# Performance work log

Measured on AMD Instinct MI355X. Metric: run time of the kernel, lower is better.

## Reference

```python
import jax, jax.numpy as jnp
import numpy as np

N_NODES = 50000
N_EDGES = 640000
IN_FEATS = 512
HID = 128
OUT_FEATS = 128
N_GRAPHS = 256


def setup_inputs() -> dict:
    key = jax.random.key(0)
    ks = jax.random.split(key, 7)
    x = jax.random.normal(ks[0], (N_NODES, IN_FEATS), dtype=jnp.float32)
    edge_index = jax.random.randint(ks[1], (2, N_EDGES), 0, N_NODES, dtype=jnp.int32)
    batch = jnp.sort(jax.random.randint(ks[2], (N_NODES,), 0, N_GRAPHS, dtype=jnp.int32))
    W1 = jax.random.normal(ks[3], (IN_FEATS, HID), dtype=jnp.float32) * (1.0 / np.sqrt(IN_FEATS))
    b1 = jnp.zeros((HID,), jnp.float32)
    W2 = jax.random.normal(ks[4], (HID, OUT_FEATS), dtype=jnp.float32) * (1.0 / np.sqrt(HID))
    b2 = jnp.zeros((OUT_FEATS,), jnp.float32)
    return {"x": x, "W1": W1, "b1": b1, "W2": W2, "b2": b2,
            "edge_index": edge_index, "batch": batch}


def reference(x, W1, b1, W2, b2, edge_index, batch):
    N = x.shape[0]
    loop = jnp.arange(N, dtype=edge_index.dtype)
    # PyG GCNConv default: add self-loops, symmetric deg^-1/2 normalization
    row = jnp.concatenate([edge_index[0], loop])  # source
    col = jnp.concatenate([edge_index[1], loop])  # target
    deg = jax.ops.segment_sum(jnp.ones_like(col, x.dtype), col, num_segments=N)
    dinv = jnp.where(deg > 0, jax.lax.rsqrt(deg), 0.0)
    norm = dinv[row] * dinv[col]  # [E+N]

    def gcn_conv(h, W, b):
        h = h @ W  # linear transform first (PyG order)
        msg = h[row] * norm[:, None]  # gather + scale
        agg = jax.ops.segment_sum(msg, col, num_segments=N)  # scatter-add
        return agg + b

    h = jax.nn.relu(gcn_conv(x, W1, b1))  # dropout is identity in eval mode
    h = gcn_conv(h, W2, b2)
    hs = jax.ops.segment_sum(h, batch, num_segments=N_GRAPHS)  # global_add_pool
    return hs, h
```

## Files before the change

kernel.cpp:

```cpp
#include <hip/hip_runtime.h>
#include <hip/hip_bf16.h>

#define N_NODES  50000
#define N_EDGES  640000
#define IN_FEATS 512
#define HID      128
#define OUT_FEATS 128
#define N_GRAPHS 256

#define SCAN_CHUNK 1024
#define SCAN_BLOCKS ((N_NODES + SCAN_CHUNK - 1) / SCAN_CHUNK)

typedef __attribute__((ext_vector_type(8))) short short8;
typedef __attribute__((ext_vector_type(4))) float f32x4;

__device__ __forceinline__ float bf2f(unsigned short u) {
    return __uint_as_float(((unsigned)u) << 16);
}
__device__ __forceinline__ unsigned short f2bf(float f) {
    __hip_bfloat16 h = __float2bfloat16(f);
    return *(unsigned short*)&h;
}


__global__ void k_count(const int* __restrict__ col, int* __restrict__ cnt) {
    int e = blockIdx.x * blockDim.x + threadIdx.x;
    if (e < N_EDGES) atomicAdd(&cnt[col[e]], 1);
}

__global__ __launch_bounds__(256) void k_scan_a(const int* __restrict__ cnt,
                                                int* __restrict__ offs,
                                                int* __restrict__ bsum) {
    __shared__ int sums[256];
    int t = threadIdx.x;
    int base = blockIdx.x * SCAN_CHUNK + t * 4;
    int c0 = 0, c1 = 0, c2 = 0, c3 = 0;
    if (base + 3 < N_NODES) {
        int4 v = *(const int4*)(cnt + base);
        c0 = v.x; c1 = v.y; c2 = v.z; c3 = v.w;
    } else {
        if (base + 0 < N_NODES) c0 = cnt[base + 0];
        if (base + 1 < N_NODES) c1 = cnt[base + 1];
        if (base + 2 < N_NODES) c2 = cnt[base + 2];
    }
    int ts = c0 + c1 + c2 + c3;
    sums[t] = ts;
    __syncthreads();
#pragma unroll
    for (int off = 1; off < 256; off <<= 1) {
        int add = (t >= off) ? sums[t - off] : 0;
        __syncthreads();
        sums[t] += add;
        __syncthreads();
    }
    int ex = sums[t] - ts;
    if (base + 3 < N_NODES) {
        int4 o;
        o.x = ex; o.y = ex + c0; o.z = ex + c0 + c1; o.w = ex + c0 + c1 + c2;
        *(int4*)(offs + base) = o;
    } else {
        if (base + 0 < N_NODES) offs[base + 0] = ex;
        if (base + 1 < N_NODES) offs[base + 1] = ex + c0;
        if (base + 2 < N_NODES) offs[base + 2] = ex + c0 + c1;
    }
    if (t == 255) bsum[blockIdx.x] = sums[255];
}

__global__ void k_scan_b(int* __restrict__ bsum, int* __restrict__ boff) {
    __shared__ int s[64];
    int t = threadIdx.x;
    int v = (t < SCAN_BLOCKS) ? bsum[t] : 0;
    s[t] = v;
    __syncthreads();
#pragma unroll
    for (int off = 1; off < 64; off <<= 1) {
        int add = (t >= off) ? s[t - off] : 0;
        __syncthreads();
        s[t] += add;
        __syncthreads();
    }
    if (t < SCAN_BLOCKS) boff[t] = s[t] - v;
}

__global__ __launch_bounds__(256) void k_scan_c(const int* __restrict__ cnt,
                                                const int* __restrict__ boff,
                                                int* __restrict__ offs,
                                                int* __restrict__ cursor,
                                                float* __restrict__ dinv) {
    int t = threadIdx.x;
    int b = blockIdx.x;
    int add = boff[b];
    int base = b * SCAN_CHUNK + t * 4;
    if (base + 3 < N_NODES) {
        int4 o = *(const int4*)(offs + base);
        o.x += add; o.y += add; o.z += add; o.w += add;
        *(int4*)(offs + base) = o;
        *(int4*)(cursor + base) = o;
        int4 c = *(const int4*)(cnt + base);
        float4 d;
        d.x = rsqrtf((float)c.x + 1.0f);
        d.y = rsqrtf((float)c.y + 1.0f);
        d.z = rsqrtf((float)c.z + 1.0f);
        d.w = rsqrtf((float)c.w + 1.0f);
        *(float4*)(dinv + base) = d;
    } else {
#pragma unroll
        for (int j = 0; j < 4; ++j) {
            int i = base + j;
            if (i < N_NODES) {
                int o = offs[i] + add;
                offs[i] = o; cursor[i] = o;
                dinv[i] = rsqrtf((float)cnt[i] + 1.0f);
            }
        }
    }
    if (b == 0 && t == 0) offs[N_NODES] = N_EDGES;
}

__global__ void k_fill(const int* __restrict__ row, const int* __restrict__ col,
                       int* __restrict__ cursor, int* __restrict__ srcIdx) {
    int e = blockIdx.x * blockDim.x + threadIdx.x;
    if (e < N_EDGES) {
        int c = col[e];
        int p = atomicAdd(&cursor[c], 1);
        srcIdx[p] = row[e];
    }
}


template <int K>
__global__ void k_cvt_wt(const float* __restrict__ W, unsigned short* __restrict__ Wt) {
    int idx = blockIdx.x * blockDim.x + threadIdx.x;
    if (idx >= K * 128) return;
    int n = idx & 127;
    int k = idx >> 7;
    Wt[(size_t)n * K + k] = f2bf(W[(size_t)k * 128 + n]);
}


template <int K>
__global__ __launch_bounds__(256) void k_gemm_mfma_f32a(const float* __restrict__ A,
                                                        const unsigned short* __restrict__ Bt,
                                                        unsigned short* __restrict__ Cb, int M) {
    __shared__ unsigned short As[4][64][8];
    __shared__ unsigned short Bs[4][128][8];
    int tid = threadIdx.x;
    int wave = tid >> 6;
    int lane = tid & 63;
    int quad = lane >> 4;
    int l15 = lane & 15;
    int m0 = blockIdx.x * 64;

    f32x4 acc[8];
#pragma unroll
    for (int nt = 0; nt < 8; ++nt) acc[nt] = (f32x4){0.f, 0.f, 0.f, 0.f};

    int gm_a = m0 + lane; if (gm_a >= M) gm_a = M - 1;
    const float* ap_base = A + (size_t)gm_a * K + wave * 8;

    for (int k0 = 0; k0 < K; k0 += 32) {
        {
            const float* ap = ap_base + k0;
            float4 v0 = *(const float4*)ap;
            float4 v1 = *(const float4*)(ap + 4);
            float f[8] = {v0.x, v0.y, v0.z, v0.w, v1.x, v1.y, v1.z, v1.w};
            short8 pk;
#pragma unroll
            for (int j = 0; j < 8; ++j) pk[j] = (short)f2bf(f[j]);
            *(short8*)&As[wave][lane][0] = pk;
        }
#pragma unroll
        for (int i = 0; i < 2; ++i) {
            int slot = tid + i * 256;
            int bkq = slot >> 7;
            int n = slot & 127;
            short8 bv = *(const short8*)(Bt + (size_t)n * K + k0 + bkq * 8);
            *(short8*)&Bs[bkq][n][0] = bv;
        }
        __syncthreads();
        short8 a = *(short8*)&As[quad][wave * 16 + l15][0];
#pragma unroll
        for (int nt = 0; nt < 8; ++nt) {
            short8 b = *(short8*)&Bs[quad][nt * 16 + l15][0];
            acc[nt] = __builtin_amdgcn_mfma_f32_16x16x32_bf16(a, b, acc[nt], 0, 0, 0);
        }
        __syncthreads();
    }
    int row_base = m0 + wave * 16 + quad * 4;
#pragma unroll
    for (int nt = 0; nt < 8; ++nt) {
#pragma unroll
        for (int r2 = 0; r2 < 4; ++r2) {
            int gm = row_base + r2;
            if (gm < M) Cb[(size_t)gm * 128 + nt * 16 + l15] = f2bf(acc[nt][r2]);
        }
    }
}


template <int K>
__global__ __launch_bounds__(256) void k_gemm_mfma_bf16a(const unsigned short* __restrict__ A,
                                                         const unsigned short* __restrict__ Bt,
                                                         unsigned short* __restrict__ Cb, int M) {
    __shared__ unsigned short As[4][64][8];
    __shared__ unsigned short Bs[4][128][8];
    int tid = threadIdx.x;
    int wave = tid >> 6;
    int lane = tid & 63;
    int quad = lane >> 4;
    int l15 = lane & 15;
    int m0 = blockIdx.x * 64;

    f32x4 acc[8];
#pragma unroll
    for (int nt = 0; nt < 8; ++nt) acc[nt] = (f32x4){0.f, 0.f, 0.f, 0.f};

    int gm_a = m0 + lane; if (gm_a >= M) gm_a = M - 1;
    const unsigned short* ap_base = A + (size_t)gm_a * K + wave * 8;

    for (int k0 = 0; k0 < K; k0 += 32) {
        *(short8*)&As[wave][lane][0] = *(const short8*)(ap_base + k0);
#pragma unroll
        for (int i = 0; i < 2; ++i) {
            int slot = tid + i * 256;
            int bkq = slot >> 7;
            int n = slot & 127;
            *(short8*)&Bs[bkq][n][0] = *(const short8*)(Bt + (size_t)n * K + k0 + bkq * 8);
        }
        __syncthreads();
        short8 a = *(short8*)&As[quad][wave * 16 + l15][0];
#pragma unroll
        for (int nt = 0; nt < 8; ++nt) {
            short8 b = *(short8*)&Bs[quad][nt * 16 + l15][0];
            acc[nt] = __builtin_amdgcn_mfma_f32_16x16x32_bf16(a, b, acc[nt], 0, 0, 0);
        }
        __syncthreads();
    }
    int row_base = m0 + wave * 16 + quad * 4;
#pragma unroll
    for (int nt = 0; nt < 8; ++nt) {
#pragma unroll
        for (int r2 = 0; r2 < 4; ++r2) {
            int gm = row_base + r2;
            if (gm < M) Cb[(size_t)gm * 128 + nt * 16 + l15] = f2bf(acc[nt][r2]);
        }
    }
}


template <int RELU, int OUTBF>
__global__ __launch_bounds__(128) void k_agg(const unsigned short* __restrict__ t,
                                             const int* __restrict__ offs,
                                             const int* __restrict__ srcIdx,
                                             const float* __restrict__ dinv,
                                             const float* __restrict__ bias,
                                             void* __restrict__ out_) {
    int i = blockIdx.x;
    int f = threadIdx.x;
    float di = dinv[i];
    float s = bf2f(t[(size_t)i * 128 + f]) * di;
    int lo = offs[i], hi = offs[i + 1];
    int e = lo;
    for (; e + 4 <= hi; e += 4) {
        int s0 = srcIdx[e + 0], s1 = srcIdx[e + 1], s2 = srcIdx[e + 2], s3 = srcIdx[e + 3];
        float d0 = dinv[s0], d1 = dinv[s1], d2 = dinv[s2], d3 = dinv[s3];
        float v0 = bf2f(t[(size_t)s0 * 128 + f]);
        float v1 = bf2f(t[(size_t)s1 * 128 + f]);
        float v2 = bf2f(t[(size_t)s2 * 128 + f]);
        float v3 = bf2f(t[(size_t)s3 * 128 + f]);
        s = fmaf(v0, d0, s); s = fmaf(v1, d1, s);
        s = fmaf(v2, d2, s); s = fmaf(v3, d3, s);
    }
    for (; e < hi; ++e) {
        int sn = srcIdx[e];
        s = fmaf(bf2f(t[(size_t)sn * 128 + f]), dinv[sn], s);
    }
    float v = s * di + bias[f];
    if (RELU) v = fmaxf(v, 0.f);
    if (OUTBF) ((unsigned short*)out_)[(size_t)i * 128 + f] = f2bf(v);
    else       ((float*)out_)[(size_t)i * 128 + f] = v;
}


__global__ void k_gstart(const int* __restrict__ batch, int* __restrict__ gstart) {
    int i = blockIdx.x * blockDim.x + threadIdx.x;
    if (i >= N_NODES) return;
    int b = batch[i];
    int bp = (i == 0) ? -1 : batch[i - 1];
    for (int g = bp + 1; g <= b; ++g) gstart[g] = i;
    if (i == N_NODES - 1) {
        for (int g = b + 1; g <= N_GRAPHS; ++g) gstart[g] = N_NODES;
    }
}

__global__ __launch_bounds__(128) void k_pool(const float* __restrict__ h,
                                              const int* __restrict__ gstart,
                                              float* __restrict__ hs) {
    int g = blockIdx.x >> 2;
    int c = blockIdx.x & 3;
    int f = threadIdx.x;
    int lo = gstart[g], hi = gstart[g + 1];
    int len = hi - lo;
    int chunk = (len + 3) >> 2;
    int r0 = lo + c * chunk;
    int r1 = r0 + chunk; if (r1 > hi) r1 = hi;
    if (r0 >= r1) return;
    float s = 0.f;
    for (int r = r0; r < r1; ++r) s += h[(size_t)r * 128 + f];
    atomicAdd(&hs[(size_t)g * 128 + f], s);
}


extern "C" void kernel_launch(void* const* d_in, const int* in_sizes, int n_in,
                              void* d_out, int out_size, void* d_ws, size_t ws_size,
                              hipStream_t stream) {
    const float* x  = (const float*)d_in[0];
    const float* W1 = (const float*)d_in[1];
    const float* b1 = (const float*)d_in[2];
    const float* W2 = (const float*)d_in[3];
    const float* b2 = (const float*)d_in[4];
    const int*   ei = (const int*)d_in[5];
    const int*   batch = (const int*)d_in[6];
    const int* row = ei;
    const int* col = ei + N_EDGES;

    float* out_hs = (float*)d_out;
    float* out_h  = (float*)d_out + N_GRAPHS * OUT_FEATS;

    char* ws = (char*)d_ws;
    unsigned short* tb   = (unsigned short*)ws;
    unsigned short* h1b  = (unsigned short*)(ws + 12800000);
    unsigned short* tb2  = (unsigned short*)(ws + 25600000);
    float* dinv = (float*)(ws + 38400000);
    int*   cnt    = (int*)(ws + 38600000);
    int*   offs   = (int*)(ws + 38800000);
    int*   cursor = (int*)(ws + 39000016);
    int*   srcIdx = (int*)(ws + 39200016);
    int*   gstart = (int*)(ws + 41760016);
    int*   bsum   = (int*)(ws + 41761056);
    int*   boff   = (int*)(ws + 41761264);
    unsigned short* wt1 = (unsigned short*)(ws + 41761472);
    unsigned short* wt2 = (unsigned short*)(ws + 41892544);

    const int TB = 256;
    hipMemsetAsync(cnt, 0, N_NODES * sizeof(int), stream);
    hipMemsetAsync(out_hs, 0, N_GRAPHS * OUT_FEATS * sizeof(float), stream);
    k_count<<<(N_EDGES + TB - 1) / TB, TB, 0, stream>>>(col, cnt);
    k_scan_a<<<SCAN_BLOCKS, 256, 0, stream>>>(cnt, offs, bsum);
    k_scan_b<<<1, 64, 0, stream>>>(bsum, boff);
    k_scan_c<<<SCAN_BLOCKS, 256, 0, stream>>>(cnt, boff, offs, cursor, dinv);
    k_fill<<<(N_EDGES + TB - 1) / TB, TB, 0, stream>>>(row, col, cursor, srcIdx);
    k_gstart<<<(N_NODES + TB - 1) / TB, TB, 0, stream>>>(batch, gstart);
    k_cvt_wt<IN_FEATS><<<(IN_FEATS * 128 + TB - 1) / TB, TB, 0, stream>>>(W1, wt1);
    k_cvt_wt<HID><<<(HID * 128 + TB - 1) / TB, TB, 0, stream>>>(W2, wt2);

    const int GB = (N_NODES + 63) / 64;
    k_gemm_mfma_f32a<IN_FEATS><<<GB, 256, 0, stream>>>(x, wt1, tb, N_NODES);
    k_agg<1, 1><<<N_NODES, 128, 0, stream>>>(tb, offs, srcIdx, dinv, b1, h1b);
    k_gemm_mfma_bf16a<HID><<<GB, 256, 0, stream>>>(h1b, wt2, tb2, N_NODES);
    k_agg<0, 0><<<N_NODES, 128, 0, stream>>>(tb2, offs, srcIdx, dinv, b2, out_h);
    k_pool<<<N_GRAPHS * 4, 128, 0, stream>>>(out_h, gstart, out_hs);
}
```

Before: 375.8 us.

## Fuse setup kernels, merge scan phases, and widen aggregation to one wave per node

Four small setup launches (gstart, weight conversions, and two memsets) are merged into a single k_prep kernel partitioned by block index. The block-sum scan is folded into k_scan_c, so each block recomputes the 64-entry prefix in shared memory. k_agg now assigns one 64-lane wave per node, with each lane handling two bf16 features via 32-bit loads, and unrolls the neighbor gather by 8 for more memory-level parallelism. The aim is to cut launch overhead and make the gather loads wider, at the cost of redundant scan work per block.

```diff
diff --git a/kernel.cpp b/kernel.cpp
--- a/kernel.cpp
+++ b/kernel.cpp
@@ -14,12 +14,51 @@
 typedef __attribute__((ext_vector_type(8))) short short8;
 typedef __attribute__((ext_vector_type(4))) float f32x4;
 
-__device__ __forceinline__ float bf2f(unsigned short u) {
-    return __uint_as_float(((unsigned)u) << 16);
+__device__ __forceinline__ float bf2f(unsigned u16) {
+    return __uint_as_float(u16 << 16);
 }
 __device__ __forceinline__ unsigned short f2bf(float f) {
     __hip_bfloat16 h = __float2bfloat16(f);
     return *(unsigned short*)&h;
+}
+
+
+#define PREP_BLOCKS 840
+
+__global__ __launch_bounds__(256) void k_prep(const float* __restrict__ W1,
+                                              const float* __restrict__ W2,
+                                              const int* __restrict__ batch,
+                                              unsigned short* __restrict__ wt1,
+                                              unsigned short* __restrict__ wt2,
+                                              int* __restrict__ cnt,
+                                              int* __restrict__ gstart,
+                                              float* __restrict__ hs) {
+    int b = blockIdx.x;
+    int t = threadIdx.x;
+    if (b < 196) {
+        int i = b * 256 + t;
+        if (i < N_NODES) {
+            int bt = batch[i];
+            int bp = (i == 0) ? -1 : batch[i - 1];
+            for (int g = bp + 1; g <= bt; ++g) gstart[g] = i;
+            if (i == N_NODES - 1)
+                for (int g = bt + 1; g <= N_GRAPHS; ++g) gstart[g] = N_NODES;
+        }
+    } else if (b < 392) {
+        int i = (b - 196) * 256 + t;
+        if (i < N_NODES) cnt[i] = 0;
+    } else if (b < 648) {
+        int idx = (b - 392) * 256 + t;
+        int n = idx & 127, k = idx >> 7;
+        wt1[(size_t)n * IN_FEATS + k] = f2bf(W1[(size_t)k * 128 + n]);
+    } else if (b < 712) {
+        int idx = (b - 648) * 256 + t;
+        int n = idx & 127, k = idx >> 7;
+        wt2[(size_t)n * HID + k] = f2bf(W2[(size_t)k * 128 + n]);
+    } else {
+        int idx = (b - 712) * 256 + t;
+        hs[idx] = 0.f;
+    }
 }
 
 
@@ -66,30 +105,25 @@
     if (t == 255) bsum[blockIdx.x] = sums[255];
 }
 
-__global__ void k_scan_b(int* __restrict__ bsum, int* __restrict__ boff) {
-    __shared__ int s[64];
-    int t = threadIdx.x;
-    int v = (t < SCAN_BLOCKS) ? bsum[t] : 0;
-    s[t] = v;
-    __syncthreads();
-#pragma unroll
-    for (int off = 1; off < 64; off <<= 1) {
-        int add = (t >= off) ? s[t - off] : 0;
-        __syncthreads();
-        s[t] += add;
-        __syncthreads();
-    }
-    if (t < SCAN_BLOCKS) boff[t] = s[t] - v;
-}
-
 __global__ __launch_bounds__(256) void k_scan_c(const int* __restrict__ cnt,
-                                                const int* __restrict__ boff,
+                                                const int* __restrict__ bsum,
                                                 int* __restrict__ offs,
                                                 int* __restrict__ cursor,
                                                 float* __restrict__ dinv) {
+    __shared__ int sb[64];
     int t = threadIdx.x;
     int b = blockIdx.x;
-    int add = boff[b];
+    if (t < 64) sb[t] = (t < SCAN_BLOCKS) ? bsum[t] : 0;
+    __syncthreads();
+#pragma unroll
+    for (int off = 1; off < 64; off <<= 1) {
+        int add = 0;
+        if (t < 64 && t >= off) add = sb[t - off];
+        __syncthreads();
+        if (t < 64) sb[t] += add;
+        __syncthreads();
+    }
+    int add = (b == 0) ? 0 : sb[b - 1];
     int base = b * SCAN_CHUNK + t * 4;
     if (base + 3 < N_NODES) {
         int4 o = *(const int4*)(offs + base);
@@ -129,16 +163,6 @@
 
 
 template <int K>
-__global__ void k_cvt_wt(const float* __restrict__ W, unsigned short* __restrict__ Wt) {
-    int idx = blockIdx.x * blockDim.x + threadIdx.x;
-    if (idx >= K * 128) return;
-    int n = idx & 127;
-    int k = idx >> 7;
-    Wt[(size_t)n * K + k] = f2bf(W[(size_t)k * 128 + n]);
-}
-
-
-template <int K>
 __global__ __launch_bounds__(256) void k_gemm_mfma_f32a(const float* __restrict__ A,
                                                         const unsigned short* __restrict__ Bt,
                                                         unsigned short* __restrict__ Cb, int M) {
@@ -174,8 +198,7 @@
             int slot = tid + i * 256;
             int bkq = slot >> 7;
             int n = slot & 127;
-            short8 bv = *(const short8*)(Bt + (size_t)n * K + k0 + bkq * 8);
-            *(short8*)&Bs[bkq][n][0] = bv;
+            *(short8*)&Bs[bkq][n][0] = *(const short8*)(Bt + (size_t)n * K + k0 + bkq * 8);
         }
         __syncthreads();
         short8 a = *(short8*)&As[quad][wave * 16 + l15][0];
@@ -249,49 +272,56 @@
 
 
 template <int RELU, int OUTBF>
-__global__ __launch_bounds__(128) void k_agg(const unsigned short* __restrict__ t,
+__global__ __launch_bounds__(128) void k_agg(const unsigned* __restrict__ t,
                                              const int* __restrict__ offs,
                                              const int* __restrict__ srcIdx,
                                              const float* __restrict__ dinv,
                                              const float* __restrict__ bias,
                                              void* __restrict__ out_) {
-    int i = blockIdx.x;
-    int f = threadIdx.x;
+    int wave = threadIdx.x >> 6;
+    int lane = threadIdx.x & 63;
+    int i = blockIdx.x * 2 + wave;
     float di = dinv[i];
-    float s = bf2f(t[(size_t)i * 128 + f]) * di;
+    unsigned self = t[(size_t)i * 64 + lane];
+    float s0 = bf2f(self & 0xffffu) * di;
+    float s1 = bf2f(self >> 16) * di;
     int lo = offs[i], hi = offs[i + 1];
     int e = lo;
-    for (; e + 4 <= hi; e += 4) {
-        int s0 = srcIdx[e + 0], s1 = srcIdx[e + 1], s2 = srcIdx[e + 2], s3 = srcIdx[e + 3];
-        float d0 = dinv[s0], d1 = dinv[s1], d2 = dinv[s2], d3 = dinv[s3];
-        float v0 = bf2f(t[(size_t)s0 * 128 + f]);
-        float v1 = bf2f(t[(size_t)s1 * 128 + f]);
-        float v2 = bf2f(t[(size_t)s2 * 128 + f]);
-        float v3 = bf2f(t[(size_t)s3 * 128 + f]);
-        s = fmaf(v0, d0, s); s = fmaf(v1, d1, s);
-        s = fmaf(v2, d2, s); s = fmaf(v3, d3, s);
+    for (; e + 8 <= hi; e += 8) {
+        int idx[8];
+#pragma unroll
+        for (int j = 0; j < 8; ++j) idx[j] = srcIdx[e + j];
+        unsigned v[8];
+#pragma unroll
+        for (int j = 0; j < 8; ++j) v[j] = t[(size_t)idx[j] * 64 + lane];
+        float d[8];
+#pragma unroll
+        for (int j = 0; j < 8; ++j) d[j] = dinv[idx[j]];
+#pragma unroll
+        for (int j = 0; j < 8; ++j) {
+            s0 = fmaf(bf2f(v[j] & 0xffffu), d[j], s0);
+            s1 = fmaf(bf2f(v[j] >> 16), d[j], s1);
+        }
     }
     for (; e < hi; ++e) {
         int sn = srcIdx[e];
-        s = fmaf(bf2f(t[(size_t)sn * 128 + f]), dinv[sn], s);
-    }
-    float v = s * di + bias[f];
-    if (RELU) v = fmaxf(v, 0.f);
-    if (OUTBF) ((unsigned short*)out_)[(size_t)i * 128 + f] = f2bf(v);
-    else       ((float*)out_)[(size_t)i * 128 + f] = v;
-}
-
-
-__global__ void k_gstart(const int* __restrict__ batch, int* __restrict__ gstart) {
-    int i = blockIdx.x * blockDim.x + threadIdx.x;
-    if (i >= N_NODES) return;
-    int b = batch[i];
-    int bp = (i == 0) ? -1 : batch[i - 1];
-    for (int g = bp + 1; g <= b; ++g) gstart[g] = i;
-    if (i == N_NODES - 1) {
-        for (int g = b + 1; g <= N_GRAPHS; ++g) gstart[g] = N_NODES;
-    }
-}
+        unsigned vv = t[(size_t)sn * 64 + lane];
+        float dd = dinv[sn];
+        s0 = fmaf(bf2f(vv & 0xffffu), dd, s0);
+        s1 = fmaf(bf2f(vv >> 16), dd, s1);
+    }
+    float2 bb = *(const float2*)(bias + lane * 2);
+    float r0 = s0 * di + bb.x;
+    float r1 = s1 * di + bb.y;
+    if (RELU) { r0 = fmaxf(r0, 0.f); r1 = fmaxf(r1, 0.f); }
+    if (OUTBF) {
+        unsigned o = (unsigned)f2bf(r0) | ((unsigned)f2bf(r1) << 16);
+        ((unsigned*)out_)[(size_t)i * 64 + lane] = o;
+    } else {
+        *(float2*)((float*)out_ + (size_t)i * 128 + lane * 2) = make_float2(r0, r1);
+    }
+}
+
 
 __global__ __launch_bounds__(128) void k_pool(const float* __restrict__ h,
                                               const int* __restrict__ gstart,
@@ -338,26 +368,20 @@
     int*   srcIdx = (int*)(ws + 39200016);
     int*   gstart = (int*)(ws + 41760016);
     int*   bsum   = (int*)(ws + 41761056);
-    int*   boff   = (int*)(ws + 41761264);
     unsigned short* wt1 = (unsigned short*)(ws + 41761472);
     unsigned short* wt2 = (unsigned short*)(ws + 41892544);
 
     const int TB = 256;
-    hipMemsetAsync(cnt, 0, N_NODES * sizeof(int), stream);
-    hipMemsetAsync(out_hs, 0, N_GRAPHS * OUT_FEATS * sizeof(float), stream);
+    k_prep<<<PREP_BLOCKS, 256, 0, stream>>>(W1, W2, batch, wt1, wt2, cnt, gstart, out_hs);
     k_count<<<(N_EDGES + TB - 1) / TB, TB, 0, stream>>>(col, cnt);
     k_scan_a<<<SCAN_BLOCKS, 256, 0, stream>>>(cnt, offs, bsum);
-    k_scan_b<<<1, 64, 0, stream>>>(bsum, boff);
-    k_scan_c<<<SCAN_BLOCKS, 256, 0, stream>>>(cnt, boff, offs, cursor, dinv);
+    k_scan_c<<<SCAN_BLOCKS, 256, 0, stream>>>(cnt, bsum, offs, cursor, dinv);
     k_fill<<<(N_EDGES + TB - 1) / TB, TB, 0, stream>>>(row, col, cursor, srcIdx);
-    k_gstart<<<(N_NODES + TB - 1) / TB, TB, 0, stream>>>(batch, gstart);
-    k_cvt_wt<IN_FEATS><<<(IN_FEATS * 128 + TB - 1) / TB, TB, 0, stream>>>(W1, wt1);
-    k_cvt_wt<HID><<<(HID * 128 + TB - 1) / TB, TB, 0, stream>>>(W2, wt2);
 
     const int GB = (N_NODES + 63) / 64;
     k_gemm_mfma_f32a<IN_FEATS><<<GB, 256, 0, stream>>>(x, wt1, tb, N_NODES);
-    k_agg<1, 1><<<N_NODES, 128, 0, stream>>>(tb, offs, srcIdx, dinv, b1, h1b);
+    k_agg<1, 1><<<N_NODES / 2, 128, 0, stream>>>((const unsigned*)tb, offs, srcIdx, dinv, b1, h1b);
     k_gemm_mfma_bf16a<HID><<<GB, 256, 0, stream>>>(h1b, wt2, tb2, N_NODES);
-    k_agg<0, 0><<<N_NODES, 128, 0, stream>>>(tb2, offs, srcIdx, dinv, b2, out_h);
+    k_agg<0, 0><<<N_NODES / 2, 128, 0, stream>>>((const unsigned*)tb2, offs, srcIdx, dinv, b2, out_h);
     k_pool<<<N_GRAPHS * 4, 128, 0, stream>>>(out_h, gstart, out_hs);
 }
```

Result: faster. 351.5 us (-6.5%).
